# Performance work log

Hardware: AMD Instinct MI355X
Metric: run time of the kernel (lower is better)

The kernel has to match this reference:

```python
import jax, jax.numpy as jnp
import numpy as np

N = 262144   # cohort size (k_n)
M = 8192     # number of ordinal anchor indices (len(Hj))


def setup_inputs() -> dict:
    key = jax.random.key(0)
    k1, k2, k3, k4, k5 = jax.random.split(key, 5)
    time = jax.random.uniform(k1, (N,), dtype=jnp.float32) * 1000.0
    event = (jax.random.uniform(k2, (N,), dtype=jnp.float32) < 0.3).astype(jnp.float32)
    y_true0 = jnp.stack([time, event], axis=1)          # [N,2] (time, event)
    y_true1 = y_true0                                    # second head labels (unused by loss)
    y_pred0 = jax.random.normal(k3, (N, 1), dtype=jnp.float32) * 0.1  # xbeta head 0
    y_pred1 = jax.random.normal(k4, (N, 1), dtype=jnp.float32) * 0.1  # xbeta head 1
    Hj = jnp.sort(jax.random.randint(k5, (M,), 0, N, dtype=jnp.int32))  # static event indices into sorted order
    log_vars = jnp.zeros((2, 1), dtype=jnp.float32)      # layer weights log_var0, log_var1
    return {"y_true0": y_true0, "y_true1": y_true1, "y_pred0": y_pred0,
            "y_pred1": y_pred1, "Hj": Hj, "log_vars": log_vars}


def reference(y_true0, y_true1, y_pred0, y_pred1, Hj, log_vars):
    n = y_true0.shape[0]
    # top_k with k = n == full descending sort by time
    _, order = jax.lax.top_k(y_true0[:, 0], n)

    # ---- neg_log_pl (Cox negative partial log-likelihood, per-sample vector) ----
    xbeta = y_pred0[order, 0]                 # [N] sorted by descending time
    event = y_true0[order, 1]                 # [N]
    denom = jnp.cumsum(jnp.exp(xbeta))        # risk-set cumulative sum
    lossA = -(event * (xbeta - jnp.log(denom)))  # [N]

    # ---- ordinal_loss0 (pairwise ranking over event indices Hj in sorted order) ----
    # intended math: for each j, for ii >= j: cost += 1 - exp(xbeta[Hj[j]] - xbeta[Hj[ii]])
    xb = y_pred1[order, 0]                    # [N] sorted
    xh = xb[Hj]                               # [M]
    m = Hj.shape[0]
    rec = 1.0 - jnp.exp(xh[:, None] - xh[None, :])   # [M,M] rec[j,ii]
    mask = jnp.triu(jnp.ones((m, m), dtype=bool))    # ii >= j
    cost2 = jnp.sum(jnp.where(mask, rec, 0.0))

    # ---- multi_loss combination with learned log variances ----
    lv0 = log_vars[0, 0]
    lv1 = log_vars[1, 0]
    precision1 = jnp.clip(jnp.exp(-lv1), 0.0, 1.0)
    loss = jnp.sum(lossA + lv0) + (precision1 * cost2 + lv1)
    return loss


if __name__ == "__main__":
    out = reference(**setup_inputs())
    print(out)
```

## Files before the change

kernel.cpp:

```cpp
#include <hip/hip_runtime.h>
#include <math.h>


#define NB (1 << 20)
#define BLK 256
#define KSL 8
#define M40 ((1ull << 40) - 1)

#define STORE_F32_A(p, v) __hip_atomic_store((p), (v), __ATOMIC_RELAXED, __HIP_MEMORY_SCOPE_AGENT)
#define STORE_U64_A(p, v) __hip_atomic_store((unsigned long long*)(p), (v), __ATOMIC_RELAXED, __HIP_MEMORY_SCOPE_AGENT)
#define LOAD_U64_A(p) __hip_atomic_load((const unsigned long long*)(p), __ATOMIC_RELAXED, __HIP_MEMORY_SCOPE_AGENT)
#define LOAD_F32_A(p) __hip_atomic_load((const float*)(p), __ATOMIC_RELAXED, __HIP_MEMORY_SCOPE_AGENT)
#define FADD_U32_A(p, v) __hip_atomic_fetch_add((p), (v), __ATOMIC_RELAXED, __HIP_MEMORY_SCOPE_AGENT)

__device__ __forceinline__ int lin_bucket(float t) {
  int b = (int)(t * 1024.0f);
  if (b < 0) b = 0;
  if (b > NB - 1) b = NB - 1;
  return b;
}

__global__ void __launch_bounds__(BLK, 4)
k_hist(const float2* __restrict__ yt0, const float* __restrict__ yp0,
       const int* __restrict__ Hj, int n, int m, int tot,
       unsigned long long* __restrict__ rec,
       unsigned long long* __restrict__ slotKE, unsigned* __restrict__ slotIdx,
       unsigned* __restrict__ bitmap) {
  int i = blockIdx.x * BLK + threadIdx.x;
  if (i < n) {
    float2 te = yt0[i];
    unsigned key = __float_as_uint(te.x);
    float e = expf(yp0[i]);
    int b = lin_bucket(te.x);
    unsigned long long qe = (unsigned long long)(e * 16777216.0f + 0.5f);
    if (qe > (1ull << 32)) qe = (1ull << 32);
    unsigned long long ret = atomicAdd(&rec[b], (1ull << 40) | qe);
    unsigned seq = (unsigned)(ret >> 40);
    if (seq < KSL) {
      size_t s = (size_t)b * KSL + seq;
      slotKE[s] = ((unsigned long long)__float_as_uint(e) << 32) | key;
      slotIdx[s] = (unsigned)i;
    }
  }
  for (int j = i; j < m; j += tot) {
    int h = Hj[j];
    atomicOr(&bitmap[h >> 5], 1u << (h & 31));
  }
}

__global__ void __launch_bounds__(BLK, 4)
k_scan(const unsigned long long* __restrict__ rec,
       unsigned long long* __restrict__ pub,
       unsigned long long* __restrict__ Epack) {
  __shared__ unsigned su[BLK];
  __shared__ float    sf[BLK];
  const int t = threadIdx.x, g = blockIdx.x;

  unsigned cK[4]; float fK[4];
  unsigned runc = 0u; float runf = 0.f;
  #pragma unroll
  for (int k = 0; k < 4; ++k) {
    int b = NB - 1 - (g * 1024 + t * 4 + k);
    unsigned long long v = rec[b];
    cK[k] = (unsigned)(v >> 40);
    fK[k] = (float)((double)(v & M40) * (1.0 / 16777216.0));
    runc += cK[k]; runf += fK[k];
  }
  su[t] = runc; sf[t] = runf;
  __syncthreads();
  for (int off2 = 1; off2 < BLK; off2 <<= 1) {
    unsigned uc = (t >= off2) ? su[t - off2] : 0u;
    float    uf = (t >= off2) ? sf[t - off2] : 0.f;
    __syncthreads();
    su[t] += uc; sf[t] += uf;
    __syncthreads();
  }
  if (t == BLK - 1)
    STORE_U64_A(&pub[g], (1ull << 63) |
                ((unsigned long long)(su[t] & 0x7FFFFFFFu) << 32) |
                (unsigned long long)__float_as_uint(sf[t]));
  unsigned thrC = (t > 0) ? su[t - 1] : 0u;
  float    thrF = (t > 0) ? sf[t - 1] : 0.f;
  __syncthreads();

  unsigned pc = 0u; float pf = 0.f;
  for (int j = t; j < g; j += BLK) {
    unsigned long long v;
    int guard = 0;
    while (!(((v = LOAD_U64_A(&pub[j])) >> 63) & 1ull)) {
      __builtin_amdgcn_s_sleep(1);
      if (++guard > 5000000) break;
    }
    pc += (unsigned)((v >> 32) & 0x7FFFFFFFu);
    pf += __uint_as_float((unsigned)v);
  }
  su[t] = pc; sf[t] = pf;
  __syncthreads();
  for (int s = BLK / 2; s > 0; s >>= 1) {
    if (t < s) { su[t] += su[t + s]; sf[t] += sf[t + s]; }
    __syncthreads();
  }
  const unsigned baseC = su[0]; const float baseF = sf[0];

  unsigned preC = 0u; float preF = 0.f;
  #pragma unroll
  for (int k = 0; k < 4; ++k) {
    int b = NB - 1 - (g * 1024 + t * 4 + k);
    unsigned sfxC = baseC + thrC + preC;
    float    sfxF = baseF + thrF + preF;
    Epack[b] = ((unsigned long long)__float_as_uint(sfxF) << 32) | sfxC;
    preC += cK[k]; preF += fK[k];
  }
}

__global__ void __launch_bounds__(BLK, 4)
k_main(const float2* __restrict__ yt0, const float* __restrict__ yp0,
       const float* __restrict__ yp1, const int* __restrict__ Hj,
       const float* __restrict__ lv, int n, int m,
       const unsigned* __restrict__ bitmap,
       const unsigned long long* __restrict__ Epack,
       const unsigned long long* __restrict__ slotKE,
       const unsigned* __restrict__ slotIdx,
       float* __restrict__ xh, double* __restrict__ accum,
       unsigned* __restrict__ doneCnt, float* __restrict__ out) {
  __shared__ double sd[BLK];
  __shared__ float  wt[4];
  __shared__ int    lastFlag;
  const int t = threadIdx.x;
  int i = blockIdx.x * BLK + t;
  double contrib = 0.0;
  if (i < n) {
    float2 te = yt0[i];
    unsigned key = __float_as_uint(te.x);
    bool evb = (te.y != 0.f);
    float e = expf(yp0[i]);
    int b = lin_bucket(te.x);
    unsigned long long ep = Epack[b];
    unsigned start = (unsigned)ep;
    float cross = __uint_as_float((unsigned)(ep >> 32));
    unsigned end = (b > 0) ? ((const unsigned*)Epack)[2u * (unsigned)(b - 1)]
                           : (unsigned)n;
    if (end > (unsigned)n) end = (unsigned)n;
    if (start > end) start = end;
    unsigned cnt = end - start;
    float wsum = 0.f;
    unsigned wcnt = 0u;
    if (cnt > 1u) {
      unsigned lim = (cnt < (unsigned)KSL) ? cnt : (unsigned)KSL;
      size_t sb = (size_t)b * KSL;
      for (unsigned s = 0; s < lim; ++s) {
        unsigned long long v = slotKE[sb + s];
        unsigned vk = (unsigned)v;
        if (vk > key) { wsum += __uint_as_float((unsigned)(v >> 32)); wcnt++; }
        else if (vk == key && slotIdx[sb + s] < (unsigned)i) {
          wsum += __uint_as_float((unsigned)(v >> 32)); wcnt++;
        }
      }
    }
    float denom = cross + wsum + e;
    int rank = (int)(start + wcnt);
    if (evb) contrib = (double)logf(denom / e);
    if ((bitmap[rank >> 5] >> (rank & 31)) & 1u) {
      int lo = 0, hi = m;
      while (lo < hi) { int mid = (lo + hi) >> 1; if (Hj[mid] < rank) lo = mid + 1; else hi = mid; }
      if (lo < m && Hj[lo] == rank) {
        float xb1 = yp1[i];
        for (int j = lo; j < m && Hj[j] == rank; ++j) STORE_F32_A(&xh[j], xb1);
      }
    }
  }
  sd[t] = contrib;
  __syncthreads();
  for (int s = 128; s > 0; s >>= 1) { if (t < s) sd[t] += sd[t + s]; __syncthreads(); }
  if (t == 0) {
    double old = atomicAdd(accum, sd[0]);
    unsigned long long ob = __double_as_longlong(old);
    asm volatile("" :: "v"(ob));
    unsigned r = FADD_U32_A(doneCnt, 1u);
    lastFlag = (r == gridDim.x - 1u) ? 1 : 0;
  }
  __syncthreads();
  if (lastFlag == 0) return;

  {
    int lane = t & 63;
    int w = t >> 6;
    double acc = 0.0;
    float carry = 0.f;
    int passes = (m + 2047) / 2048;
    for (int pss = passes - 1; pss >= 0; --pss) {
      int base = pss * 2048 + t * 8;
      float x[8], eb[8];
      float c = 0.f;
      #pragma unroll
      for (int k = 0; k < 8; ++k) {
        int j = base + k;
        x[k] = (j < m) ? LOAD_F32_A(&xh[j]) : 0.f;
        eb[k] = (j < m) ? expf(-x[k]) : 0.f;
        c += eb[k];
      }
      float s = c;
      #pragma unroll
      for (int d = 1; d < 64; d <<= 1) {
        float o = __shfl_down(s, d, 64);
        if (lane + d < 64) s += o;
      }
      float wtot = __shfl(s, 0, 64);
      if (lane == 0) wt[w] = wtot;
      __syncthreads();
      float after = 0.f, ptot = 0.f;
      #pragma unroll
      for (int w2 = 0; w2 < 4; ++w2) { ptot += wt[w2]; if (w2 > w) after += wt[w2]; }
      float S = (s - c) + after + carry;
      #pragma unroll
      for (int k = 7; k >= 0; --k) {
        int j = base + k;
        S += eb[k];
        if (j < m) acc += (double)(expf(x[k]) * S);
      }
      __syncthreads();
      carry += ptot;
    }
    sd[t] = acc;
    __syncthreads();
    for (int s2 = 128; s2 > 0; s2 >>= 1) { if (t < s2) sd[t] += sd[t + s2]; __syncthreads(); }
    if (t == 0) {
      double T = (double)m * (double)(m + 1) * 0.5;
      double cost2 = T - sd[0];
      float lv0 = lv[0], lv1 = lv[1];
      float prec1 = fminf(expf(-lv1), 1.0f);
      double av = __longlong_as_double((long long)LOAD_U64_A(accum));
      double loss = av + (double)n * (double)lv0 + (double)prec1 * cost2 + (double)lv1;
      out[0] = (float)loss;
    }
  }
}

extern "C" void kernel_launch(void* const* d_in, const int* in_sizes, int n_in,
                              void* d_out, int out_size, void* d_ws, size_t ws_size,
                              hipStream_t stream) {
  (void)n_in; (void)out_size;
  const float2* yt0 = (const float2*)d_in[0];
  const float*  yp0 = (const float*)d_in[2];
  const float*  yp1 = (const float*)d_in[3];
  const int*    Hj  = (const int*)d_in[4];
  const float*  lv  = (const float*)d_in[5];
  int n = in_sizes[0] / 2;
  int m = in_sizes[4];

  char* ws = (char*)d_ws;
  size_t off = 0;
  auto alloc = [&](size_t bytes) -> void* {
    void* p = ws + off;
    off += (bytes + 255) & ~(size_t)255;
    return p;
  };
  double*   accum   = (double*)alloc(128);
  unsigned* doneCnt = (unsigned*)alloc(128);
  size_t nbm = ((size_t)(n + 31) / 32) * 4;
  unsigned* bitmap  = (unsigned*)alloc(nbm);
  unsigned long long* pub = (unsigned long long*)alloc(1024 * 8);
  unsigned long long* rec = (unsigned long long*)alloc((size_t)NB * 8);
  size_t zbytes = off;
  unsigned long long* Epack  = (unsigned long long*)alloc((size_t)NB * 8);
  unsigned long long* slotKE = (unsigned long long*)alloc((size_t)NB * KSL * 8);
  unsigned*           slotIdx= (unsigned*)alloc((size_t)NB * KSL * 4);
  float*    xh      = (float*)alloc((size_t)m * 4);
  if (off > ws_size) return;

  hipMemsetAsync(ws, 0, zbytes, stream);

  int gN = (n + BLK - 1) / BLK;
  int tot = gN * BLK;
  k_hist<<<dim3(gN), dim3(BLK), 0, stream>>>(yt0, yp0, Hj, n, m, tot,
                                             rec, slotKE, slotIdx, bitmap);
  k_scan<<<dim3(NB / 1024), dim3(BLK), 0, stream>>>(rec, pub, Epack);
  k_main<<<dim3(gN), dim3(BLK), 0, stream>>>(yt0, yp0, yp1, Hj, lv, n, m,
                                             bitmap, Epack, slotKE, slotIdx,
                                             xh, accum, doneCnt,
                                             (float*)d_out);
}
```

Measured before the change: 128.9 us.

## Replace fixed-slot bucket storage with counting-sort scatter and fewer buckets

Cuts the bucket count from 1M to 256K and drops the fixed 8-slot-per-bucket arrays. k_hist now records each element's sequence number within its bucket, and a new k_scatter kernel writes key/exp/index into a compact array at the scanned bucket offset. k_main then scans the whole bucket span to find the within-bucket rank. This shrinks the slot workspace and the scan over 1M buckets, and it removes the 8-element overflow limit. In exchange it adds a kernel launch and makes buckets larger, so the per-element scan in k_main gets longer.

```diff
diff --git a/kernel.cpp b/kernel.cpp
--- a/kernel.cpp
+++ b/kernel.cpp
@@ -2,9 +2,8 @@
 #include <math.h>
 
 
-#define NB (1 << 20)
+#define NB (1 << 18)
 #define BLK 256
-#define KSL 8
 #define M40 ((1ull << 40) - 1)
 
 #define STORE_F32_A(p, v) __hip_atomic_store((p), (v), __ATOMIC_RELAXED, __HIP_MEMORY_SCOPE_AGENT)
@@ -14,7 +13,7 @@
 #define FADD_U32_A(p, v) __hip_atomic_fetch_add((p), (v), __ATOMIC_RELAXED, __HIP_MEMORY_SCOPE_AGENT)
 
 __device__ __forceinline__ int lin_bucket(float t) {
-  int b = (int)(t * 1024.0f);
+  int b = (int)(t * 256.0f);
   if (b < 0) b = 0;
   if (b > NB - 1) b = NB - 1;
   return b;
@@ -23,24 +22,17 @@
 __global__ void __launch_bounds__(BLK, 4)
 k_hist(const float2* __restrict__ yt0, const float* __restrict__ yp0,
        const int* __restrict__ Hj, int n, int m, int tot,
-       unsigned long long* __restrict__ rec,
-       unsigned long long* __restrict__ slotKE, unsigned* __restrict__ slotIdx,
+       unsigned long long* __restrict__ rec, unsigned* __restrict__ seq,
        unsigned* __restrict__ bitmap) {
   int i = blockIdx.x * BLK + threadIdx.x;
   if (i < n) {
     float2 te = yt0[i];
-    unsigned key = __float_as_uint(te.x);
     float e = expf(yp0[i]);
     int b = lin_bucket(te.x);
     unsigned long long qe = (unsigned long long)(e * 16777216.0f + 0.5f);
     if (qe > (1ull << 32)) qe = (1ull << 32);
     unsigned long long ret = atomicAdd(&rec[b], (1ull << 40) | qe);
-    unsigned seq = (unsigned)(ret >> 40);
-    if (seq < KSL) {
-      size_t s = (size_t)b * KSL + seq;
-      slotKE[s] = ((unsigned long long)__float_as_uint(e) << 32) | key;
-      slotIdx[s] = (unsigned)i;
-    }
+    seq[i] = (unsigned)(ret >> 40);
   }
   for (int j = i; j < m; j += tot) {
     int h = Hj[j];
@@ -114,13 +106,33 @@
 }
 
 __global__ void __launch_bounds__(BLK, 4)
+k_scatter(const float2* __restrict__ yt0, const float* __restrict__ yp0, int n,
+          const unsigned* __restrict__ seq,
+          const unsigned long long* __restrict__ Epack,
+          uint2* __restrict__ skey2, unsigned* __restrict__ sidx) {
+  int i = blockIdx.x * BLK + threadIdx.x;
+  if (i >= n) return;
+  float2 te = yt0[i];
+  unsigned key = __float_as_uint(te.x);
+  int b = lin_bucket(te.x);
+  const unsigned* E32 = (const unsigned*)Epack;
+  unsigned start = E32[2u * (unsigned)b];
+  unsigned end = (b > 0) ? E32[2u * (unsigned)(b - 1)] : (unsigned)n;
+  if (end - start < 2u) return;
+  float e = expf(yp0[i]);
+  unsigned pos = start + seq[i];
+  uint2 v; v.x = key; v.y = __float_as_uint(e);
+  skey2[pos] = v;
+  sidx[pos] = (unsigned)i;
+}
+
+__global__ void __launch_bounds__(BLK, 4)
 k_main(const float2* __restrict__ yt0, const float* __restrict__ yp0,
        const float* __restrict__ yp1, const int* __restrict__ Hj,
        const float* __restrict__ lv, int n, int m,
        const unsigned* __restrict__ bitmap,
        const unsigned long long* __restrict__ Epack,
-       const unsigned long long* __restrict__ slotKE,
-       const unsigned* __restrict__ slotIdx,
+       const uint2* __restrict__ skey2, const unsigned* __restrict__ sidx,
        float* __restrict__ xh, double* __restrict__ accum,
        unsigned* __restrict__ doneCnt, float* __restrict__ out) {
   __shared__ double sd[BLK];
@@ -142,18 +154,14 @@
                            : (unsigned)n;
     if (end > (unsigned)n) end = (unsigned)n;
     if (start > end) start = end;
-    unsigned cnt = end - start;
     float wsum = 0.f;
     unsigned wcnt = 0u;
-    if (cnt > 1u) {
-      unsigned lim = (cnt < (unsigned)KSL) ? cnt : (unsigned)KSL;
-      size_t sb = (size_t)b * KSL;
-      for (unsigned s = 0; s < lim; ++s) {
-        unsigned long long v = slotKE[sb + s];
-        unsigned vk = (unsigned)v;
-        if (vk > key) { wsum += __uint_as_float((unsigned)(v >> 32)); wcnt++; }
-        else if (vk == key && slotIdx[sb + s] < (unsigned)i) {
-          wsum += __uint_as_float((unsigned)(v >> 32)); wcnt++;
+    if (end - start > 1u) {
+      for (unsigned q = start; q < end; ++q) {
+        uint2 v = skey2[q];
+        if (v.x > key) { wsum += __uint_as_float(v.y); wcnt++; }
+        else if (v.x == key && sidx[q] < (unsigned)i) {
+          wsum += __uint_as_float(v.y); wcnt++;
         }
       }
     }
@@ -259,13 +267,14 @@
   unsigned* doneCnt = (unsigned*)alloc(128);
   size_t nbm = ((size_t)(n + 31) / 32) * 4;
   unsigned* bitmap  = (unsigned*)alloc(nbm);
-  unsigned long long* pub = (unsigned long long*)alloc(1024 * 8);
+  unsigned long long* pub = (unsigned long long*)alloc((NB / 1024) * 8);
   unsigned long long* rec = (unsigned long long*)alloc((size_t)NB * 8);
   size_t zbytes = off;
-  unsigned long long* Epack  = (unsigned long long*)alloc((size_t)NB * 8);
-  unsigned long long* slotKE = (unsigned long long*)alloc((size_t)NB * KSL * 8);
-  unsigned*           slotIdx= (unsigned*)alloc((size_t)NB * KSL * 4);
-  float*    xh      = (float*)alloc((size_t)m * 4);
+  unsigned long long* Epack = (unsigned long long*)alloc((size_t)NB * 8);
+  unsigned* seq   = (unsigned*)alloc((size_t)n * 4);
+  uint2*    skey2 = (uint2*)alloc((size_t)n * 8);
+  unsigned* sidx  = (unsigned*)alloc((size_t)n * 4);
+  float*    xh    = (float*)alloc((size_t)m * 4);
   if (off > ws_size) return;
 
   hipMemsetAsync(ws, 0, zbytes, stream);
@@ -273,10 +282,12 @@
   int gN = (n + BLK - 1) / BLK;
   int tot = gN * BLK;
   k_hist<<<dim3(gN), dim3(BLK), 0, stream>>>(yt0, yp0, Hj, n, m, tot,
-                                             rec, slotKE, slotIdx, bitmap);
+                                             rec, seq, bitmap);
   k_scan<<<dim3(NB / 1024), dim3(BLK), 0, stream>>>(rec, pub, Epack);
+  k_scatter<<<dim3(gN), dim3(BLK), 0, stream>>>(yt0, yp0, n, seq, Epack,
+                                                skey2, sidx);
   k_main<<<dim3(gN), dim3(BLK), 0, stream>>>(yt0, yp0, yp1, Hj, lv, n, m,
-                                             bitmap, Epack, slotKE, slotIdx,
+                                             bitmap, Epack, skey2, sidx,
                                              xh, accum, doneCnt,
                                              (float*)d_out);
 }
```

Result: no change. 128.5 us (-0.4%).
